# Optimization experiments

Hardware: AMD Instinct MI355X
Metric: run time of the kernel (lower is better)

The kernel has to match this reference:

```python
import jax, jax.numpy as jnp
import numpy as np

N = 8192
D_IN = 128
D_OUT = 128


def setup_inputs() -> dict:
    key = jax.random.key(0)
    k1, k2, k3, k4 = jax.random.split(key, 4)
    x = jax.random.normal(k1, (N, D_IN), dtype=jnp.float32)
    adj = jax.random.uniform(k2, (N, N), dtype=jnp.float32)
    # nn.Linear params: weight [out, in], bias [out]
    bound = 1.0 / np.sqrt(D_IN)
    W = jax.random.uniform(k3, (D_OUT, D_IN), minval=-bound, maxval=bound, dtype=jnp.float32)
    b = jax.random.uniform(k4, (D_OUT,), minval=-bound, maxval=bound, dtype=jnp.float32)
    return {"x": x, "adj": adj, "W": W, "b": b}


def reference(x, adj, W, b):
    # Symmetric normalization: D^{-1/2} A D^{-1/2}, expressed as fused
    # row/col scaling instead of materializing diagonal matrices.
    rowsum = adj.sum(axis=1)                      # [N]
    d_inv_sqrt = jnp.power(rowsum, -0.5)
    d_inv_sqrt = jnp.where(jnp.isinf(d_inv_sqrt), 0.0, d_inv_sqrt)
    adj_norm = d_inv_sqrt[:, None] * adj * d_inv_sqrt[None, :]  # [N, N]
    h = adj_norm @ x                              # [N, D_IN]
    return h @ W.T + b                            # [N, D_OUT]
```

## Files before the change

kernel.cpp:

```cpp
#include <hip/hip_runtime.h>
#include <hip/hip_bf16.h>

typedef short bf16x8 __attribute__((ext_vector_type(8)));
typedef float f32x16 __attribute__((ext_vector_type(16)));
typedef float f32x4v __attribute__((ext_vector_type(4)));

#define GN 8192
#define GD 128
#define KSPLIT 8


__global__ __launch_bounds__(256) void k_rowcvt(const float* __restrict__ adj,
                                                float* __restrict__ s,
                                                __hip_bfloat16* __restrict__ adjb) {
  const int row = blockIdx.x;
  const int t = threadIdx.x;
  const f32x4v* p = (const f32x4v*)(adj + (size_t)row * GN);
  f32x4v v[8];
  float acc = 0.f;
#pragma unroll
  for (int i = 0; i < 8; ++i) {
    v[i] = __builtin_nontemporal_load(p + t + i * 256);
    acc += (v[i].x + v[i].y) + (v[i].z + v[i].w);
  }
#pragma unroll
  for (int off = 32; off > 0; off >>= 1) acc += __shfl_down(acc, off, 64);
  __shared__ float red[4];
  __shared__ float sbc;
  if ((t & 63) == 0) red[t >> 6] = acc;
  __syncthreads();
  if (t == 0) {
    float tot = (red[0] + red[1]) + (red[2] + red[3]);
    float sc = (tot > 0.f) ? rsqrtf(tot) : 0.f;
    sbc = sc;
    s[row] = sc;
  }
  __syncthreads();
  const float sc = sbc;
  __hip_bfloat16* orow = adjb + (size_t)row * GN;
#pragma unroll
  for (int i = 0; i < 8; ++i) {
    __hip_bfloat16 hb[4];
    hb[0] = __float2bfloat16(v[i].x * sc);
    hb[1] = __float2bfloat16(v[i].y * sc);
    hb[2] = __float2bfloat16(v[i].z * sc);
    hb[3] = __float2bfloat16(v[i].w * sc);
    *(uint2*)(orow + (size_t)(t + i * 256) * 4) = *(uint2*)hb;
  }
}

__global__ __launch_bounds__(256) void k_packy(const float* __restrict__ x,
                                               const float* __restrict__ s,
                                               const float* __restrict__ W,
                                               __hip_bfloat16* __restrict__ yp) {
  __shared__ __align__(16) __hip_bfloat16 Xs[64 * 136];
  __shared__ __align__(16) __hip_bfloat16 Ws[128 * 136];
  __shared__ __align__(16) __hip_bfloat16 Yp[128 * 72];
  __shared__ float sv[64];
  const int kb = blockIdx.x;
  const int t = threadIdx.x;
  if (t < 64) sv[t] = s[kb * 64 + t];
  __syncthreads();
  const float4* xp = (const float4*)(x + (size_t)kb * 64 * GD);
#pragma unroll
  for (int j = 0; j < 8; ++j) {
    int i = t + j * 256;
    int r = i >> 5, c4 = i & 31;
    float4 v = xp[i];
    float sc = sv[r];
    __hip_bfloat16 hb[4];
    hb[0] = __float2bfloat16(v.x * sc);
    hb[1] = __float2bfloat16(v.y * sc);
    hb[2] = __float2bfloat16(v.z * sc);
    hb[3] = __float2bfloat16(v.w * sc);
    *(uint2*)(Xs + r * 136 + c4 * 4) = *(uint2*)hb;
  }
#pragma unroll
  for (int j = 0; j < 16; ++j) {
    int i = t + j * 256;
    int o = i >> 5, k4 = i & 31;
    float4 w = *(const float4*)(W + (size_t)o * GD + k4 * 4);
    __hip_bfloat16 hb[4];
    hb[0] = __float2bfloat16(w.x);
    hb[1] = __float2bfloat16(w.y);
    hb[2] = __float2bfloat16(w.z);
    hb[3] = __float2bfloat16(w.w);
    *(uint2*)(Ws + o * 136 + k4 * 4) = *(uint2*)hb;
  }
  __syncthreads();
  const int lane = t & 63;
  const int wave = t >> 6;
  const int mtile = wave & 1;
  const int n0 = (wave >> 1) * 2;
  const int koff = (lane >> 5) * 8;
  const int arow = mtile * 32 + (lane & 31);
  f32x16 acc0, acc1;
#pragma unroll
  for (int i = 0; i < 16; ++i) { acc0[i] = 0.f; acc1[i] = 0.f; }
#pragma unroll
  for (int kk = 0; kk < 128; kk += 16) {
    bf16x8 af = *(const bf16x8*)(Xs + arow * 136 + kk + koff);
    bf16x8 b0 = *(const bf16x8*)(Ws + (n0 * 32 + (lane & 31)) * 136 + kk + koff);
    bf16x8 b1 = *(const bf16x8*)(Ws + ((n0 + 1) * 32 + (lane & 31)) * 136 + kk + koff);
    acc0 = __builtin_amdgcn_mfma_f32_32x32x16_bf16(af, b0, acc0, 0, 0, 0);
    acc1 = __builtin_amdgcn_mfma_f32_32x32x16_bf16(af, b1, acc1, 0, 0, 0);
  }
#pragma unroll
  for (int reg = 0; reg < 16; ++reg) {
    int kkl = mtile * 32 + (reg & 3) + 8 * (reg >> 2) + 4 * (lane >> 5);
    int c0 = n0 * 32 + (lane & 31);
    Yp[c0 * 72 + kkl] = __float2bfloat16(acc0[reg]);
    Yp[(c0 + 32) * 72 + kkl] = __float2bfloat16(acc1[reg]);
  }
  __syncthreads();
  const uint4* srcv = (const uint4*)Yp;
  uint4* dstv = (uint4*)((char*)yp + (size_t)kb * 18432);
  for (int i = t; i < 1152; i += 256) dstv[i] = srcv[i];
}

__global__ __launch_bounds__(256, 2) void k_gemm(const __hip_bfloat16* __restrict__ adjb,
                                                 const __hip_bfloat16* __restrict__ yp,
                                                 float* __restrict__ part) {
  __shared__ __align__(16) __hip_bfloat16 Asm[128 * 72];
  __shared__ __align__(16) __hip_bfloat16 Bsm[128 * 72];
  const int mb = blockIdx.x;
  const int ks = blockIdx.y;
  const int t = threadIdx.x;
  const int lane = t & 63;
  const int wave = t >> 6;
  const int wm = wave >> 1, wn = wave & 1;

  f32x16 acc00, acc01, acc10, acc11;
#pragma unroll
  for (int i = 0; i < 16; ++i) {
    acc00[i] = 0.f; acc01[i] = 0.f; acc10[i] = 0.f; acc11[i] = 0.f;
  }

  const int ar = t >> 1;
  const int ah = (t & 1) * 32;
  const __hip_bfloat16* arow = adjb + (size_t)(mb * 128 + ar) * GN + ks * 1024 + ah;
  const char* bsrc_base = (const char*)yp + (size_t)(ks * 16) * 18432;

  const int a_lds_off = ar * 72 + ah;
  const int afrag_row = wm * 64 + (lane & 31);
  const int koff = (lane >> 5) * 8;
  const int bcol0 = wn * 64 + (lane & 31);

  for (int kt = 0; kt < 16; ++kt) {
    {
      const char* bg = bsrc_base + (size_t)kt * 18432;
#pragma unroll
      for (int c = 0; c < 5; ++c) {
        int chunk = wave + c * 4;
        if (chunk < 18) {
          __builtin_amdgcn_global_load_lds(
              (const __attribute__((address_space(1))) unsigned int*)(bg + chunk * 1024 + lane * 16),
              (__attribute__((address_space(3))) unsigned int*)((char*)Bsm + chunk * 1024),
              16, 0, 0);
        }
      }
    }
    {
      const uint4* s4 = (const uint4*)(arow + (size_t)kt * 64);
      uint4 q0 = s4[0], q1 = s4[1], q2 = s4[2], q3 = s4[3];
      uint4* d = (uint4*)(Asm + a_lds_off);
      d[0] = q0; d[1] = q1; d[2] = q2; d[3] = q3;
    }
    __syncthreads();
#pragma unroll
    for (int kk = 0; kk < 64; kk += 16) {
      bf16x8 a0 = *(const bf16x8*)(Asm + afrag_row * 72 + kk + koff);
      bf16x8 a1 = *(const bf16x8*)(Asm + (afrag_row + 32) * 72 + kk + koff);
      bf16x8 b0 = *(const bf16x8*)(Bsm + bcol0 * 72 + kk + koff);
      bf16x8 b1 = *(const bf16x8*)(Bsm + (bcol0 + 32) * 72 + kk + koff);
      acc00 = __builtin_amdgcn_mfma_f32_32x32x16_bf16(a0, b0, acc00, 0, 0, 0);
      acc01 = __builtin_amdgcn_mfma_f32_32x32x16_bf16(a0, b1, acc01, 0, 0, 0);
      acc10 = __builtin_amdgcn_mfma_f32_32x32x16_bf16(a1, b0, acc10, 0, 0, 0);
      acc11 = __builtin_amdgcn_mfma_f32_32x32x16_bf16(a1, b1, acc11, 0, 0, 0);
    }
    __syncthreads();
  }

  float* pb = part + (size_t)ks * GN * GD + (size_t)(mb * 128) * GD;
#pragma unroll
  for (int reg = 0; reg < 16; ++reg) {
    int r0 = wm * 64 + (reg & 3) + 8 * (reg >> 2) + 4 * (lane >> 5);
    int c0 = wn * 64 + (lane & 31);
    pb[(size_t)r0 * GD + c0] = acc00[reg];
    pb[(size_t)r0 * GD + c0 + 32] = acc01[reg];
    pb[(size_t)(r0 + 32) * GD + c0] = acc10[reg];
    pb[(size_t)(r0 + 32) * GD + c0 + 32] = acc11[reg];
  }
}

__global__ __launch_bounds__(256) void k_red(const float* __restrict__ part,
                                             const float* __restrict__ b,
                                             float* __restrict__ out) {
  __shared__ float4 bs4[32];
  const int t = threadIdx.x;
  if (t < 32) bs4[t] = ((const float4*)b)[t];
  __syncthreads();
  const int row0 = blockIdx.x * 32;
#pragma unroll
  for (int j = 0; j < 4; ++j) {
    int i = t + j * 256;
    int r = i >> 5, c4 = i & 31;
    size_t idx = (size_t)(row0 + r) * GD + c4 * 4;
    float4 a = bs4[c4];
#pragma unroll
    for (int ksl = 0; ksl < KSPLIT; ++ksl) {
      float4 p = *(const float4*)(part + idx + (size_t)ksl * GN * GD);
      a.x += p.x; a.y += p.y; a.z += p.z; a.w += p.w;
    }
    *(float4*)(out + idx) = a;
  }
}

extern "C" void kernel_launch(void* const* d_in, const int* in_sizes, int n_in,
                              void* d_out, int out_size, void* d_ws, size_t ws_size,
                              hipStream_t stream) {
  const float* x   = (const float*)d_in[0];
  const float* adj = (const float*)d_in[1];
  const float* W   = (const float*)d_in[2];
  const float* b   = (const float*)d_in[3];
  float* out = (float*)d_out;

  float* s = (float*)d_ws;
  __hip_bfloat16* yp   = (__hip_bfloat16*)((char*)d_ws + 32768);
  __hip_bfloat16* adjb = (__hip_bfloat16*)((char*)d_ws + 2392064);
  float* part = (float*)((char*)d_ws + 136609792);

  k_rowcvt<<<8192, 256, 0, stream>>>(adj, s, adjb);
  k_packy<<<128, 256, 0, stream>>>(x, s, W, yp);
  k_gemm<<<dim3(64, KSPLIT), 256, 0, stream>>>(adjb, yp, part);
  k_red<<<256, 256, 0, stream>>>(part, b, out);
}
```

Baseline: 398.6 us.

## Double-buffer GEMM LDS tiles with direct global-to-LDS loads and XOR swizzle

The split-K GEMM now double-buffers its A and B shared-memory tiles, prefetching the next k-tile while MFMAs run on the current one, and drops one barrier per iteration. The A tile now uses global_load_lds direct copies instead of going through registers. Padded LDS layouts are replaced by an XOR swizzle (also applied to the packed Y layout) to avoid bank conflicts with less LDS padding. LDS use per block doubles to 64 KB, which may limit the two-blocks-per-CU occupancy.

```diff
diff --git a/kernel.cpp b/kernel.cpp
--- a/kernel.cpp
+++ b/kernel.cpp
@@ -55,7 +55,7 @@
                                                __hip_bfloat16* __restrict__ yp) {
   __shared__ __align__(16) __hip_bfloat16 Xs[64 * 136];
   __shared__ __align__(16) __hip_bfloat16 Ws[128 * 136];
-  __shared__ __align__(16) __hip_bfloat16 Yp[128 * 72];
+  __shared__ __align__(16) __hip_bfloat16 Yp[128 * 64];
   __shared__ float sv[64];
   const int kb = blockIdx.x;
   const int t = threadIdx.x;
@@ -109,26 +109,31 @@
   for (int reg = 0; reg < 16; ++reg) {
     int kkl = mtile * 32 + (reg & 3) + 8 * (reg >> 2) + 4 * (lane >> 5);
     int c0 = n0 * 32 + (lane & 31);
-    Yp[c0 * 72 + kkl] = __float2bfloat16(acc0[reg]);
-    Yp[(c0 + 32) * 72 + kkl] = __float2bfloat16(acc1[reg]);
+    int xr = (c0 & 7) << 4;
+    *(__hip_bfloat16*)((char*)Yp + ((c0 * 128 + kkl * 2) ^ xr)) = __float2bfloat16(acc0[reg]);
+    *(__hip_bfloat16*)((char*)Yp + (((c0 + 32) * 128 + kkl * 2) ^ xr)) = __float2bfloat16(acc1[reg]);
   }
   __syncthreads();
   const uint4* srcv = (const uint4*)Yp;
-  uint4* dstv = (uint4*)((char*)yp + (size_t)kb * 18432);
-  for (int i = t; i < 1152; i += 256) dstv[i] = srcv[i];
+  uint4* dstv = (uint4*)((char*)yp + (size_t)kb * 16384);
+  for (int i = t; i < 1024; i += 256) dstv[i] = srcv[i];
 }
 
 __global__ __launch_bounds__(256, 2) void k_gemm(const __hip_bfloat16* __restrict__ adjb,
                                                  const __hip_bfloat16* __restrict__ yp,
                                                  float* __restrict__ part) {
-  __shared__ __align__(16) __hip_bfloat16 Asm[128 * 72];
-  __shared__ __align__(16) __hip_bfloat16 Bsm[128 * 72];
+  __shared__ __align__(16) __hip_bfloat16 Asm[2][8192];
+  __shared__ __align__(16) __hip_bfloat16 Bsm[2][8192];
   const int mb = blockIdx.x;
   const int ks = blockIdx.y;
   const int t = threadIdx.x;
   const int lane = t & 63;
   const int wave = t >> 6;
   const int wm = wave >> 1, wn = wave & 1;
+  const int l31 = lane & 31;
+  const int koff = (lane >> 5) * 8;
+  const int bxor = (l31 & 7) << 4;
+  const int cid0 = wave * 4;
 
   f32x16 acc00, acc01, acc10, acc11;
 #pragma unroll
@@ -136,56 +141,59 @@
     acc00[i] = 0.f; acc01[i] = 0.f; acc10[i] = 0.f; acc11[i] = 0.f;
   }
 
-  const int ar = t >> 1;
-  const int ah = (t & 1) * 32;
-  const __hip_bfloat16* arow = adjb + (size_t)(mb * 128 + ar) * GN + ks * 1024 + ah;
-  const char* bsrc_base = (const char*)yp + (size_t)(ks * 16) * 18432;
-
-  const int a_lds_off = ar * 72 + ah;
-  const int afrag_row = wm * 64 + (lane & 31);
-  const int koff = (lane >> 5) * 8;
-  const int bcol0 = wn * 64 + (lane & 31);
+  const int arow0 = cid0 * 8 + (lane >> 3);
+  const int acol = ((lane & 7) ^ ((lane >> 3) & 7)) * 8;
+  const __hip_bfloat16* aSrc0 = adjb + (size_t)(mb * 128 + arow0) * GN + ks * 1024 + acol;
+  const char* bSrc0 = (const char*)yp + (size_t)(ks * 16) * 16384 + cid0 * 1024 + lane * 16;
+
+#define STAGE(dbuf, kt_) do {                                                              \
+    const __hip_bfloat16* as_ = aSrc0 + (kt_) * 64;                                        \
+    const char* bs_ = bSrc0 + (size_t)(kt_) * 16384;                                       \
+    _Pragma("unroll")                                                                      \
+    for (int i_ = 0; i_ < 4; ++i_) {                                                       \
+      __builtin_amdgcn_global_load_lds(                                                    \
+          (const __attribute__((address_space(1))) unsigned int*)(as_ + (size_t)i_ * 8 * GN), \
+          (__attribute__((address_space(3))) unsigned int*)(&Asm[dbuf][(cid0 + i_) * 512]),   \
+          16, 0, 0);                                                                       \
+      __builtin_amdgcn_global_load_lds(                                                    \
+          (const __attribute__((address_space(1))) unsigned int*)(bs_ + i_ * 1024),        \
+          (__attribute__((address_space(3))) unsigned int*)((char*)Bsm[dbuf] + (cid0 + i_) * 1024), \
+          16, 0, 0);                                                                       \
+    }                                                                                      \
+  } while (0)
+
+  STAGE(0, 0);
+  __syncthreads();
+
+  const int aoff = (wm * 64 + l31) * 128;
+  const int boff = (wn * 64 + l31) * 128;
 
   for (int kt = 0; kt < 16; ++kt) {
-    {
-      const char* bg = bsrc_base + (size_t)kt * 18432;
-#pragma unroll
-      for (int c = 0; c < 5; ++c) {
-        int chunk = wave + c * 4;
-        if (chunk < 18) {
-          __builtin_amdgcn_global_load_lds(
-              (const __attribute__((address_space(1))) unsigned int*)(bg + chunk * 1024 + lane * 16),
-              (__attribute__((address_space(3))) unsigned int*)((char*)Bsm + chunk * 1024),
-              16, 0, 0);
-        }
-      }
-    }
-    {
-      const uint4* s4 = (const uint4*)(arow + (size_t)kt * 64);
-      uint4 q0 = s4[0], q1 = s4[1], q2 = s4[2], q3 = s4[3];
-      uint4* d = (uint4*)(Asm + a_lds_off);
-      d[0] = q0; d[1] = q1; d[2] = q2; d[3] = q3;
-    }
-    __syncthreads();
+    const int cur = kt & 1;
+    if (kt < 15) STAGE(cur ^ 1, kt + 1);
+    const char* Ab = (const char*)Asm[cur] + aoff;
+    const char* Bb = (const char*)Bsm[cur] + boff;
 #pragma unroll
     for (int kk = 0; kk < 64; kk += 16) {
-      bf16x8 a0 = *(const bf16x8*)(Asm + afrag_row * 72 + kk + koff);
-      bf16x8 a1 = *(const bf16x8*)(Asm + (afrag_row + 32) * 72 + kk + koff);
-      bf16x8 b0 = *(const bf16x8*)(Bsm + bcol0 * 72 + kk + koff);
-      bf16x8 b1 = *(const bf16x8*)(Bsm + (bcol0 + 32) * 72 + kk + koff);
+      const int off = ((kk + koff) * 2) ^ bxor;
+      bf16x8 a0 = *(const bf16x8*)(Ab + off);
+      bf16x8 a1 = *(const bf16x8*)(Ab + 4096 + off);
+      bf16x8 b0 = *(const bf16x8*)(Bb + off);
+      bf16x8 b1 = *(const bf16x8*)(Bb + 4096 + off);
       acc00 = __builtin_amdgcn_mfma_f32_32x32x16_bf16(a0, b0, acc00, 0, 0, 0);
       acc01 = __builtin_amdgcn_mfma_f32_32x32x16_bf16(a0, b1, acc01, 0, 0, 0);
       acc10 = __builtin_amdgcn_mfma_f32_32x32x16_bf16(a1, b0, acc10, 0, 0, 0);
       acc11 = __builtin_amdgcn_mfma_f32_32x32x16_bf16(a1, b1, acc11, 0, 0, 0);
     }
-    __syncthreads();
-  }
+    if (kt < 15) __syncthreads();
+  }
+#undef STAGE
 
   float* pb = part + (size_t)ks * GN * GD + (size_t)(mb * 128) * GD;
 #pragma unroll
   for (int reg = 0; reg < 16; ++reg) {
     int r0 = wm * 64 + (reg & 3) + 8 * (reg >> 2) + 4 * (lane >> 5);
-    int c0 = wn * 64 + (lane & 31);
+    int c0 = wn * 64 + l31;
     pb[(size_t)r0 * GD + c0] = acc00[reg];
     pb[(size_t)r0 * GD + c0 + 32] = acc01[reg];
     pb[(size_t)(r0 + 32) * GD + c0] = acc10[reg];
@@ -227,8 +235,8 @@
 
   float* s = (float*)d_ws;
   __hip_bfloat16* yp   = (__hip_bfloat16*)((char*)d_ws + 32768);
-  __hip_bfloat16* adjb = (__hip_bfloat16*)((char*)d_ws + 2392064);
-  float* part = (float*)((char*)d_ws + 136609792);
+  __hip_bfloat16* adjb = (__hip_bfloat16*)((char*)d_ws + 2129920);
+  float* part = (float*)((char*)d_ws + 136347648);
 
   k_rowcvt<<<8192, 256, 0, stream>>>(adj, s, adjb);
   k_packy<<<128, 256, 0, stream>>>(x, s, W, yp);
```

Result: no change. 398.7 us (+0.0%).
